# Kernel tuning notes

Hardware: AMD Instinct MI355X
Metric: run time of the kernel (lower is better)

The kernel has to match this reference:

```python
import jax, jax.numpy as jnp
import numpy as np

B, S, D, H = 4, 2048, 128, 8

def setup_inputs() -> dict:
    key = jax.random.key(0)
    ks = jax.random.split(key, 11)
    sc_in = 1.0 / np.sqrt(D)
    sc_out = 1.0 / np.sqrt(H * D)
    return {
        "Q": jax.random.normal(ks[0], (B, S, D), jnp.float32),
        "K": jax.random.normal(ks[1], (B, S, D), jnp.float32),
        "V": jax.random.normal(ks[2], (B, S, D), jnp.float32),
        "WQ_w": jax.random.normal(ks[3], (H * D, D), jnp.float32) * sc_in,
        "WQ_b": jax.random.normal(ks[4], (H * D,), jnp.float32) * 0.01,
        "WK_w": jax.random.normal(ks[5], (H * D, D), jnp.float32) * sc_in,
        "WK_b": jax.random.normal(ks[6], (H * D,), jnp.float32) * 0.01,
        "WV_w": jax.random.normal(ks[7], (H * D, D), jnp.float32) * sc_in,
        "WV_b": jax.random.normal(ks[8], (H * D,), jnp.float32) * 0.01,
        "W_w": jax.random.normal(ks[9], (D, H * D), jnp.float32) * sc_out,
        "W_b": jax.random.normal(ks[10], (D,), jnp.float32) * 0.01,
    }

def reference(Q, K, V, WQ_w, WQ_b, WK_w, WK_b, WV_w, WV_b, W_w, W_b):
    b, s, d = Q.shape
    h = WQ_w.shape[0] // d
    # Linear projections: [b,s,d] -> [b,s,h*d] -> [b,h,s,d]
    rQ = (Q @ WQ_w.T + WQ_b).reshape(b, s, h, d).transpose(0, 2, 1, 3)
    rK = (K @ WK_w.T + WK_b).reshape(b, s, h, d).transpose(0, 2, 1, 3)
    rV = (V @ WV_w.T + WV_b).reshape(b, s, h, d).transpose(0, 2, 1, 3)
    # Scores: [b,h,s,s], scaled by sqrt(head_dim) = sqrt(input_dim)
    scores = jnp.einsum("bhqd,bhkd->bhqk", rQ, rK) / jnp.sqrt(jnp.asarray(d, rQ.dtype))
    sim = jax.nn.softmax(scores, axis=-1)
    # Attend and merge heads: [b,h,s,d] -> [b,s,h*d]
    oV = jnp.einsum("bhqk,bhkd->bqhd", sim, rV).reshape(b, s, h * d)
    return oV @ W_w.T + W_b
```

## Files before the change

kernel.cpp:

```cpp
#include <hip/hip_runtime.h>
#include <hip/hip_bf16.h>

typedef unsigned short u16;
typedef unsigned int   u32;
typedef short v8s __attribute__((ext_vector_type(8)));
typedef float v4f __attribute__((ext_vector_type(4)));
typedef float v16f __attribute__((ext_vector_type(16)));

#define MFMA16(a,b,c) __builtin_amdgcn_mfma_f32_16x16x32_bf16(a,b,c,0,0,0)
#define MFMA32(a,b,c) __builtin_amdgcn_mfma_f32_32x32x16_bf16(a,b,c,0,0,0)


__device__ __forceinline__ u16 f2b(float f){ u32 i; __builtin_memcpy(&i,&f,4); u32 r = (i + 0x7FFFu + ((i>>16)&1u))>>16; return (u16)r; }
__device__ __forceinline__ u32 pk2(float a, float b){
  __hip_bfloat162 h = __float22bfloat162_rn(make_float2(a,b));
  u32 r; __builtin_memcpy(&r,&h,4); return r;
}

__device__ __forceinline__ void gl16(const void* g, void* l){
  __builtin_amdgcn_global_load_lds((const __attribute__((address_space(1))) u32*)g,
                                   (__attribute__((address_space(3))) u32*)l, 16, 0, 0);
}

__device__ __forceinline__ void stage8f(const float* g, u16* l){
  float4 a = *(const float4*)g, b = *(const float4*)(g+4);
  uint4 q;
  q.x = pk2(a.x, a.y); q.y = pk2(a.z, a.w);
  q.z = pk2(b.x, b.y); q.w = pk2(b.z, b.w);
  *(uint4*)l = q;
}

__global__ __launch_bounds__(256) void proj_qkv(
    const float* __restrict__ Qx, const float* __restrict__ Kx, const float* __restrict__ Vx,
    const float* __restrict__ WQw, const float* __restrict__ WQb,
    const float* __restrict__ WKw, const float* __restrict__ WKb,
    const float* __restrict__ WVw, const float* __restrict__ WVb,
    u16* __restrict__ Qp, u16* __restrict__ Kp, u16* __restrict__ Vt)
{
  __shared__ u16 smem[32768];
  u16* As = smem;
  u16* Ws = smem + 16384;

  const int z = blockIdx.z;
  const float* X    = (z==0) ? Qx  : (z==1 ? Kx  : Vx);
  const float* W    = (z==0) ? WQw : (z==1 ? WKw : WVw);
  const float* bias = (z==0) ? WQb : (z==1 ? WKb : WVb);
  u16* out          = (z==0) ? Qp  : (z==1 ? Kp  : Vt);
  const float qs    = (z==0) ? 0.12751743076f : 1.0f;

  const int tid = threadIdx.x, wv = tid>>6, lane = tid&63;
  const int quad = lane>>4, l16 = lane&15;
  const int r4 = lane>>2, c4 = lane&3;
  const int m0 = blockIdx.x*128, n0 = blockIdx.y*128;

  for (int idx = wv; idx < 32; idx += 4) {
    int kt = idx >> 3, rg = idx & 7;
    int row = rg*16 + r4;
    stage8f(X + (size_t)(m0+row)*128 + kt*32 + c4*8, &As[kt*4096 + rg*512 + lane*8]);
    stage8f(W + (size_t)(n0+row)*128 + kt*32 + c4*8, &Ws[kt*4096 + rg*512 + lane*8]);
  }
  __syncthreads();

  const int wm = wv & 1, wn = wv >> 1;
  v4f acc[4][4];
#pragma unroll
  for (int i=0;i<4;i++)
#pragma unroll
    for (int j=0;j<4;j++) acc[i][j] = (v4f){0.f,0.f,0.f,0.f};

  if (z < 2) {
#pragma unroll
    for (int ks=0; ks<4; ++ks) {
      v8s af[4], bf[4];
#pragma unroll
      for (int mi=0; mi<4; ++mi) af[mi] = *(const v8s*)&As[ks*4096 + (wm*64+mi*16+l16)*32 + quad*8];
#pragma unroll
      for (int ni=0; ni<4; ++ni) bf[ni] = *(const v8s*)&Ws[ks*4096 + (wn*64+ni*16+l16)*32 + quad*8];
#pragma unroll
      for (int mi=0; mi<4; ++mi)
#pragma unroll
        for (int ni=0; ni<4; ++ni)
          acc[mi][ni] = MFMA16(bf[ni], af[mi], acc[mi][ni]);
    }
#pragma unroll
    for (int ni=0; ni<4; ++ni) {
      int nb = n0 + wn*64 + ni*16 + quad*4;
      float bv0 = bias[nb+0]*qs;
      float bv1 = bias[nb+1]*qs;
      float bv2 = bias[nb+2]*qs;
      float bv3 = bias[nb+3]*qs;
      int h = n0 >> 7, dh = nb & 127;
#pragma unroll
      for (int mi=0; mi<4; ++mi) {
        int m = m0 + wm*64 + mi*16 + l16;
        int b = m >> 11, s = m & 2047;
        uint2 pk;
        pk.x = pk2(fmaf(acc[mi][ni][0], qs, bv0), fmaf(acc[mi][ni][1], qs, bv1));
        pk.y = pk2(fmaf(acc[mi][ni][2], qs, bv2), fmaf(acc[mi][ni][3], qs, bv3));
        *(uint2*)&out[(size_t)(((b<<3) + h)*2048 + s)*128 + dh] = pk;
      }
    }
  } else {
#pragma unroll
    for (int ks=0; ks<4; ++ks) {
      v8s af[4], bf[4];
#pragma unroll
      for (int mi=0; mi<4; ++mi) af[mi] = *(const v8s*)&As[ks*4096 + (wm*64+mi*16+l16)*32 + quad*8];
#pragma unroll
      for (int ni=0; ni<4; ++ni) bf[ni] = *(const v8s*)&Ws[ks*4096 + (wn*64+ni*16+l16)*32 + quad*8];
#pragma unroll
      for (int mi=0; mi<4; ++mi)
#pragma unroll
        for (int ni=0; ni<4; ++ni)
          acc[mi][ni] = MFMA16(af[mi], bf[ni], acc[mi][ni]);
    }
    __syncthreads();
    u16* Cs = smem;
#pragma unroll
    for (int ni=0; ni<4; ++ni) {
      int nl = wn*64 + ni*16 + l16;
      float bv = bias[n0 + nl];
#pragma unroll
      for (int mi=0; mi<4; ++mi) {
        int ml = wm*64 + mi*16 + quad*4;
        uint2 pk;
        pk.x = pk2(acc[mi][ni][0] + bv, acc[mi][ni][1] + bv);
        pk.y = pk2(acc[mi][ni][2] + bv, acc[mi][ni][3] + bv);
        *(uint2*)&Cs[nl*136 + ml] = pk;
      }
    }
    __syncthreads();
    const int nl = tid >> 1;
    const int mb = (tid & 1) * 64;
    const int h = (n0 + nl) >> 7, dh = (n0 + nl) & 127;
    const int b = m0 >> 11, s0 = m0 & 2047;
    size_t gbase = (((size_t)((b<<3) + h)*128 + dh)*2048) + s0 + mb;
    size_t lbase = (size_t)nl*136 + mb;
#pragma unroll
    for (int j = 0; j < 8; ++j)
      *(uint4*)&out[gbase + j*8] = *(const uint4*)&Cs[lbase + j*8];
  }
}

__global__ __launch_bounds__(256, 2) void attn(
    const u16* __restrict__ Qp, const u16* __restrict__ Kp,
    const u16* __restrict__ Vt, u16* __restrict__ O)
{
  __shared__ u16 smem[32768];

  const int tid = threadIdx.x, wv = tid>>6, lane = tid&63;
  const int l32 = lane&31, h = lane>>5;

  const int n  = blockIdx.x;
  const int bh = (n&7)*4 + (n>>7);
  const int q0 = ((n>>3)&15) * 128;

  const u16* Qb = Qp + (size_t)bh*262144 + (size_t)q0*128;
  const u16* Kb = Kp + (size_t)bh*262144;
  const u16* Vb = Vt + (size_t)bh*262144;

  for (int r = 0; r < 8; ++r) {
    int idx = r*256 + tid;
    int kd = idx>>8, q = (idx>>1)&127, hh = idx&1;
    gl16(Qb + q*128 + kd*16 + hh*8, &smem[idx*8]);
  }
  __syncthreads();
  const int qrow = wv*32 + l32;
  v8s qf[8];
#pragma unroll
  for (int kd = 0; kd < 8; ++kd)
    qf[kd] = *(const v8s*)&smem[kd*2048 + qrow*16 + h*8];
  __syncthreads();

  int gK[4], gV[4], lK[4], lV[4];
#pragma unroll
  for (int r = 0; r < 4; ++r) {
    int idx = r*256 + tid;
    lK[r] = idx*8;  lV[r] = 16384 + idx*8;
    int key = idx>>4, pcK = idx&15;
    gK[r] = key*128 + ((pcK ^ (key&15)))*8;
    int d = idx>>3, pcV = idx&7;
    gV[r] = d*2048 + ((pcV ^ (d&7)))*8;
  }
  int kfo[8], vfo[4];
#pragma unroll
  for (int kd = 0; kd < 8; ++kd) kfo[kd] = ((kd*2 + h) ^ (l32 & 15)) * 8;
#pragma unroll
  for (int kt = 0; kt < 4; ++kt) vfo[kt] = ((kt*2 + h) ^ (l32 & 7)) * 8;

  v8s onesf;
#pragma unroll
  for (int j = 0; j < 8; ++j) onesf[j] = (short)0x3F80;

  v16f oacc[4], lacc;
#pragma unroll
  for (int nt = 0; nt < 4; ++nt)
#pragma unroll
    for (int j = 0; j < 16; ++j) oacc[nt][j] = 0.f;
#pragma unroll
  for (int j = 0; j < 16; ++j) lacc[j] = 0.f;

#pragma unroll
  for (int r = 0; r < 4; ++r) gl16(Kb + gK[r], &smem[lK[r]]);
#pragma unroll
  for (int r = 0; r < 4; ++r) gl16(Vb + gV[r], &smem[lV[r]]);

  for (int it = 0; it < 32; ++it) {
    const int cur = it & 1;
    const int ko = cur*8192;
    const int vo = cur*8192;
    __syncthreads();

    if (it + 1 < 32) {
      const u16* Kt  = Kb + (it+1)*8192;
      const u16* Vtt = Vb + (it+1)*64;
      const int po = (cur^1)*8192;
#pragma unroll
      for (int r = 0; r < 4; ++r) gl16(Kt  + gK[r], &smem[po + lK[r]]);
#pragma unroll
      for (int r = 0; r < 4; ++r) gl16(Vtt + gV[r], &smem[po + lV[r] - 16384 + 16384]);
    }

    v16f sa[2];
#pragma unroll
    for (int m = 0; m < 2; ++m)
#pragma unroll
      for (int j = 0; j < 16; ++j) sa[m][j] = 0.f;
#pragma unroll
    for (int kd = 0; kd < 8; ++kd) {
#pragma unroll
      for (int m = 0; m < 2; ++m) {
        v8s kf = *(const v8s*)&smem[ko + (m*32 + l32)*128 + kfo[kd]];
        sa[m] = MFMA32(kf, qf[kd], sa[m]);
      }
    }

    u32 P32[2][4][2];
#pragma unroll
    for (int m = 0; m < 2; ++m)
#pragma unroll
      for (int g = 0; g < 4; ++g) {
        P32[m][g][0] = pk2(__builtin_amdgcn_exp2f(sa[m][g*4+0]),
                           __builtin_amdgcn_exp2f(sa[m][g*4+1]));
        P32[m][g][1] = pk2(__builtin_amdgcn_exp2f(sa[m][g*4+2]),
                           __builtin_amdgcn_exp2f(sa[m][g*4+3]));
      }

    v8s pf[4];
#pragma unroll
    for (int kt = 0; kt < 4; ++kt) {
      const int m = kt >> 1, e = (kt & 1) * 2, o = e + 1;
      u32 t0 = h ? P32[m][e][0] : P32[m][o][0];
      u32 t1 = h ? P32[m][e][1] : P32[m][o][1];
      u32 r0 = (u32)__shfl_xor((int)t0, 32);
      u32 r1 = (u32)__shfl_xor((int)t1, 32);
      union { u32 u[4]; v8s s; } f;
      f.u[0] = h ? r0 : P32[m][e][0];
      f.u[1] = h ? r1 : P32[m][e][1];
      f.u[2] = h ? P32[m][o][0] : r0;
      f.u[3] = h ? P32[m][o][1] : r1;
      pf[kt] = f.s;
    }

#pragma unroll
    for (int kt = 0; kt < 4; ++kt) {
      lacc = MFMA32(pf[kt], onesf, lacc);
#pragma unroll
      for (int nt = 0; nt < 4; ++nt) {
        v8s vf = *(const v8s*)&smem[16384 + vo + (nt*32 + l32)*64 + vfo[kt]];
        oacc[nt] = MFMA32(pf[kt], vf, oacc[nt]);
      }
    }
  }

  const int b = bh >> 3, hd = bh & 7;
#pragma unroll
  for (int reg = 0; reg < 16; ++reg) {
    int q = q0 + wv*32 + (reg&3) + 8*(reg>>2) + 4*h;
    float inv = 1.0f / lacc[reg];
    size_t base = ((size_t)(b*2048 + q))*1024 + hd*128;
#pragma unroll
    for (int nt = 0; nt < 4; ++nt)
      O[base + nt*32 + l32] = f2b(oacc[nt][reg] * inv);
  }
}

__global__ __launch_bounds__(256) void outproj(
    const u16* __restrict__ A, const float* __restrict__ Ww,
    const float* __restrict__ Wb, float* __restrict__ out)
{
  __shared__ u16 As[2048];
  __shared__ u16 Ws[8192];

  const int tid = threadIdx.x, wv = tid>>6, lane = tid&63;
  const int quad = lane>>4, l16 = lane&15;
  const int r4 = lane>>2, c4 = lane&3;
  const int m0 = blockIdx.x*32;

  v4f acc[2][2];
#pragma unroll
  for (int i=0;i<2;i++)
#pragma unroll
    for (int j=0;j<2;j++) acc[i][j] = (v4f){0.f,0.f,0.f,0.f};

  for (int kb = 0; kb < 1024; kb += 64) {
    {
      int kt = wv >> 1, rg = wv & 1;
      int row = rg*16 + r4;
      gl16(A + (size_t)(m0+row)*1024 + kb + kt*32 + c4*8, &As[kt*1024 + rg*512 + lane*8]);
    }
    for (int idx = wv; idx < 16; idx += 4) {
      int kt = idx >> 3, rg = idx & 7;
      int row = rg*16 + r4;
      stage8f(Ww + (size_t)row*1024 + kb + kt*32 + c4*8, &Ws[kt*4096 + rg*512 + lane*8]);
    }
    __syncthreads();
#pragma unroll
    for (int ks = 0; ks < 2; ++ks) {
      v8s af0 = *(const v8s*)&As[ks*1024 + (l16)*32 + quad*8];
      v8s af1 = *(const v8s*)&As[ks*1024 + (16 + l16)*32 + quad*8];
#pragma unroll
      for (int nj = 0; nj < 2; ++nj) {
        v8s bf = *(const v8s*)&Ws[ks*4096 + ((wv*2+nj)*16 + l16)*32 + quad*8];
        acc[0][nj] = MFMA16(af0, bf, acc[0][nj]);
        acc[1][nj] = MFMA16(af1, bf, acc[1][nj]);
      }
    }
    __syncthreads();
  }

#pragma unroll
  for (int nj = 0; nj < 2; ++nj) {
    int col = (wv*2+nj)*16 + l16;
    float bv = Wb[col];
#pragma unroll
    for (int mi = 0; mi < 2; ++mi) {
#pragma unroll
      for (int r = 0; r < 4; ++r) {
        int row = m0 + mi*16 + quad*4 + r;
        out[(size_t)row*128 + col] = acc[mi][nj][r] + bv;
      }
    }
  }
}

extern "C" void kernel_launch(void* const* d_in, const int* in_sizes, int n_in,
                              void* d_out, int out_size, void* d_ws, size_t ws_size,
                              hipStream_t stream) {
  const float* Q   = (const float*)d_in[0];
  const float* K   = (const float*)d_in[1];
  const float* V   = (const float*)d_in[2];
  const float* WQw = (const float*)d_in[3];
  const float* WQb = (const float*)d_in[4];
  const float* WKw = (const float*)d_in[5];
  const float* WKb = (const float*)d_in[6];
  const float* WVw = (const float*)d_in[7];
  const float* WVb = (const float*)d_in[8];
  const float* Ww  = (const float*)d_in[9];
  const float* Wb  = (const float*)d_in[10];
  u16* ws = (u16*)d_ws;

  const size_t SZ = (size_t)4*8*2048*128;
  u16* Qp = ws;
  u16* Kp = Qp + SZ;
  u16* Vt = Kp + SZ;
  u16* Ow = Vt + SZ;

  hipLaunchKernelGGL(proj_qkv, dim3(64,8,3), dim3(256), 0, stream,
                     Q,K,V,WQw,WQb,WKw,WKb,WVw,WVb,Qp,Kp,Vt);
  hipLaunchKernelGGL(attn, dim3(512), dim3(256), 0, stream, Qp,Kp,Vt,Ow);
  hipLaunchKernelGGL(outproj, dim3(256), dim3(256), 0, stream, Ow, Ww, Wb, (float*)d_out);
}
```

Measured before the change: 211.9 us.

## Double-buffer outproj LDS, use permlane32 swap for P, prioritize MFMA waves

The output projection kernel now uses two LDS buffers. The next K-slice is staged while the current one is consumed, which removes one barrier per iteration. In the attention kernel, the half-wave exchange of the exponentiated score fragments uses v_permlane32_swap instead of two __shfl_xor plus selects, cutting LDS-crossbar permute traffic. s_setprio raises wave priority around the QK and PV MFMA blocks to favour matrix issue. The double buffer doubles outproj's LDS footprint, which could lower occupancy.

```diff
diff --git a/kernel.cpp b/kernel.cpp
--- a/kernel.cpp
+++ b/kernel.cpp
@@ -6,6 +6,7 @@
 typedef short v8s __attribute__((ext_vector_type(8)));
 typedef float v4f __attribute__((ext_vector_type(4)));
 typedef float v16f __attribute__((ext_vector_type(16)));
+typedef int   v2i __attribute__((ext_vector_type(2)));
 
 #define MFMA16(a,b,c) __builtin_amdgcn_mfma_f32_16x16x32_bf16(a,b,c,0,0,0)
 #define MFMA32(a,b,c) __builtin_amdgcn_mfma_f32_32x32x16_bf16(a,b,c,0,0,0)
@@ -226,6 +227,7 @@
     for (int m = 0; m < 2; ++m)
 #pragma unroll
       for (int j = 0; j < 16; ++j) sa[m][j] = 0.f;
+    __builtin_amdgcn_s_setprio(1);
 #pragma unroll
     for (int kd = 0; kd < 8; ++kd) {
 #pragma unroll
@@ -234,6 +236,7 @@
         sa[m] = MFMA32(kf, qf[kd], sa[m]);
       }
     }
+    __builtin_amdgcn_s_setprio(0);
 
     u32 P32[2][4][2];
 #pragma unroll
@@ -250,18 +253,23 @@
 #pragma unroll
     for (int kt = 0; kt < 4; ++kt) {
       const int m = kt >> 1, e = (kt & 1) * 2, o = e + 1;
-      u32 t0 = h ? P32[m][e][0] : P32[m][o][0];
-      u32 t1 = h ? P32[m][e][1] : P32[m][o][1];
-      u32 r0 = (u32)__shfl_xor((int)t0, 32);
-      u32 r1 = (u32)__shfl_xor((int)t1, 32);
       union { u32 u[4]; v8s s; } f;
-      f.u[0] = h ? r0 : P32[m][e][0];
-      f.u[1] = h ? r1 : P32[m][e][1];
-      f.u[2] = h ? P32[m][o][0] : r0;
-      f.u[3] = h ? P32[m][o][1] : r1;
+#if __has_builtin(__builtin_amdgcn_permlane32_swap)
+      v2i r0 = __builtin_amdgcn_permlane32_swap((int)P32[m][e][0], (int)P32[m][o][0], false, false);
+      v2i r1 = __builtin_amdgcn_permlane32_swap((int)P32[m][e][1], (int)P32[m][o][1], false, false);
+      f.u[0] = (u32)r0[0]; f.u[1] = (u32)r1[0];
+      f.u[2] = (u32)r0[1]; f.u[3] = (u32)r1[1];
+#else
+      u32 a0 = P32[m][e][0], b0 = P32[m][o][0];
+      u32 a1 = P32[m][e][1], b1 = P32[m][o][1];
+      asm("v_permlane32_swap_b32 %0, %1" : "+v"(a0), "+v"(b0));
+      asm("v_permlane32_swap_b32 %0, %1" : "+v"(a1), "+v"(b1));
+      f.u[0] = a0; f.u[1] = a1; f.u[2] = b0; f.u[3] = b1;
+#endif
       pf[kt] = f.s;
     }
 
+    __builtin_amdgcn_s_setprio(1);
 #pragma unroll
     for (int kt = 0; kt < 4; ++kt) {
       lacc = MFMA32(pf[kt], onesf, lacc);
@@ -271,6 +279,7 @@
         oacc[nt] = MFMA32(pf[kt], vf, oacc[nt]);
       }
     }
+    __builtin_amdgcn_s_setprio(0);
   }
 
   const int b = bh >> 3, hd = bh & 7;
@@ -289,8 +298,8 @@
     const u16* __restrict__ A, const float* __restrict__ Ww,
     const float* __restrict__ Wb, float* __restrict__ out)
 {
-  __shared__ u16 As[2048];
-  __shared__ u16 Ws[8192];
+  __shared__ u16 As[2][2048];
+  __shared__ u16 Ws[2][8192];
 
   const int tid = threadIdx.x, wv = tid>>6, lane = tid&63;
   const int quad = lane>>4, l16 = lane&15;
@@ -303,30 +312,35 @@
 #pragma unroll
     for (int j=0;j<2;j++) acc[i][j] = (v4f){0.f,0.f,0.f,0.f};
 
-  for (int kb = 0; kb < 1024; kb += 64) {
+  auto stage = [&](int kb, int buf) {
     {
       int kt = wv >> 1, rg = wv & 1;
       int row = rg*16 + r4;
-      gl16(A + (size_t)(m0+row)*1024 + kb + kt*32 + c4*8, &As[kt*1024 + rg*512 + lane*8]);
+      gl16(A + (size_t)(m0+row)*1024 + kb + kt*32 + c4*8, &As[buf][kt*1024 + rg*512 + lane*8]);
     }
     for (int idx = wv; idx < 16; idx += 4) {
       int kt = idx >> 3, rg = idx & 7;
       int row = rg*16 + r4;
-      stage8f(Ww + (size_t)row*1024 + kb + kt*32 + c4*8, &Ws[kt*4096 + rg*512 + lane*8]);
-    }
+      stage8f(Ww + (size_t)row*1024 + kb + kt*32 + c4*8, &Ws[buf][kt*4096 + rg*512 + lane*8]);
+    }
+  };
+
+  stage(0, 0);
+  for (int kb = 0; kb < 1024; kb += 64) {
+    const int cur = (kb >> 6) & 1;
     __syncthreads();
+    if (kb + 64 < 1024) stage(kb + 64, cur ^ 1);
 #pragma unroll
     for (int ks = 0; ks < 2; ++ks) {
-      v8s af0 = *(const v8s*)&As[ks*1024 + (l16)*32 + quad*8];
-      v8s af1 = *(const v8s*)&As[ks*1024 + (16 + l16)*32 + quad*8];
+      v8s af0 = *(const v8s*)&As[cur][ks*1024 + (l16)*32 + quad*8];
+      v8s af1 = *(const v8s*)&As[cur][ks*1024 + (16 + l16)*32 + quad*8];
 #pragma unroll
       for (int nj = 0; nj < 2; ++nj) {
-        v8s bf = *(const v8s*)&Ws[ks*4096 + ((wv*2+nj)*16 + l16)*32 + quad*8];
+        v8s bf = *(const v8s*)&Ws[cur][ks*4096 + ((wv*2+nj)*16 + l16)*32 + quad*8];
         acc[0][nj] = MFMA16(af0, bf, acc[0][nj]);
         acc[1][nj] = MFMA16(af1, bf, acc[1][nj]);
       }
     }
-    __syncthreads();
   }
 
 #pragma unroll
```

Result: faster. 207.6 us (-2.0%).
